# Kernel tuning notes

Hardware: AMD Instinct MI355X
Metric: run time of the kernel (lower is better)

Reference implementation:

```python
import jax, jax.numpy as jnp
import numpy as np

N_QUBITS = 8
N_LAYERS = 4
BATCH = 4096


def _ry(theta):
    # RY(theta) = [[cos(t/2), -sin(t/2)], [sin(t/2), cos(t/2)]]
    c = jnp.cos(theta / 2).astype(jnp.complex64)
    s = jnp.sin(theta / 2).astype(jnp.complex64)
    return jnp.stack([jnp.stack([c, -s], axis=-1),
                      jnp.stack([s, c], axis=-1)], axis=-2)  # (..., 2, 2)


def _rz(theta):
    # RZ(theta) = diag(exp(-i t/2), exp(+i t/2))
    p = jnp.exp(-0.5j * theta.astype(jnp.complex64))
    z = jnp.zeros_like(p)
    return jnp.stack([jnp.stack([p, z], axis=-1),
                      jnp.stack([z, jnp.conj(p)], axis=-1)], axis=-2)


def _apply_1q(state, U, w):
    # state: (B, 2, 2, ..., 2); apply 2x2 unitary U on wire w (axis 1+w).
    st = jnp.moveaxis(state, 1 + w, -1)
    if U.ndim == 3:  # per-sample (batched) gate, U: (B, 2, 2)
        st = jnp.einsum('bij,b...j->b...i', U, st)
    else:            # shared gate, U: (2, 2)
        st = jnp.einsum('ij,b...j->b...i', U, st)
    return jnp.moveaxis(st, -1, 1 + w)


def _apply_cnot(state, c, t):
    # flip target wire t where control wire c is |1>
    st = jnp.moveaxis(state, (1 + c, 1 + t), (-2, -1))
    st = jnp.concatenate([st[..., 0:1, :], st[..., 1:2, ::-1]], axis=-2)
    return jnp.moveaxis(st, (-2, -1), (1 + c, 1 + t))


def _circuit(x, weights):
    B = x.shape[0]
    state = jnp.zeros((B,) + (2,) * N_QUBITS, jnp.complex64)
    state = state.at[(slice(None),) + (0,) * N_QUBITS].set(1.0)  # |0...0>
    # Angle encoding: RY(x_i) on each wire, batched over samples
    for i in range(N_QUBITS):
        state = _apply_1q(state, _ry(x[:, i]), i)
    # Variational layers: CNOT ring then RY/RZ rotations
    for l in range(N_LAYERS):
        for i in range(N_QUBITS):
            state = _apply_cnot(state, i, (i + 1) % N_QUBITS)
        for i in range(N_QUBITS):
            state = _apply_1q(state, _ry(weights[l, i, 0]), i)
            state = _apply_1q(state, _rz(weights[l, i, 1]), i)
    # <Z_0> = P(q0=0) - P(q0=1)
    probs = jnp.sum(jnp.abs(state.reshape(B, 2, -1)) ** 2, axis=-1)
    return (probs[:, 0] - probs[:, 1]).astype(jnp.float32)


def setup_inputs() -> dict:
    key = jax.random.key(0)
    k1, k2 = jax.random.split(key)
    x = jax.random.uniform(k1, (BATCH, N_QUBITS), dtype=jnp.float32) * jnp.pi
    weights = jax.random.normal(k2, (N_LAYERS, N_QUBITS, 2), dtype=jnp.float32) * 0.1
    return {"x": x, "weights": weights}


def reference(x, weights):
    return _circuit(x, weights)
```

## Files before the change

### kernel.cpp

```cpp
#include <hip/hip_runtime.h>

#define NQ 8
#define NL 4
#define BATCH 4096


template <int CTRL>
__device__ __forceinline__ float dppx(float v) {
  return __int_as_float(
      __builtin_amdgcn_update_dpp(0, __float_as_int(v), CTRL, 0xF, 0xF, true));
}

template <int MASK>
__device__ __forceinline__ float swzx(float v) {
  return __int_as_float(
      __builtin_amdgcn_ds_swizzle(__float_as_int(v), (MASK << 10) | 0x1F));
}

__device__ __forceinline__ float xor32(float v) { return __shfl_xor(v, 32, 64); }

template <int W>
__device__ __forceinline__ float xl(float v) {
  if constexpr (W == 0) return xor32(v);
  else if constexpr (W == 1) return swzx<16>(v);
  else if constexpr (W == 2) return dppx<0x128>(v);
  else if constexpr (W == 3) return swzx<4>(v);
  else if constexpr (W == 4) return dppx<0x4E>(v);
  else return dppx<0xB1>(v);
}

template <int W>
__device__ __forceinline__ void ry_gate(float re[4], float im[4],
                                        float c, float s, int lane) {
  if constexpr (W <= 5) {
    const float ss = ((lane >> (5 - W)) & 1) ? s : -s;
    float pr[4], pi[4];
#pragma unroll
    for (int r = 0; r < 4; ++r) { pr[r] = xl<W>(re[r]); pi[r] = xl<W>(im[r]); }
#pragma unroll
    for (int r = 0; r < 4; ++r) {
      re[r] = c * re[r] + ss * pr[r];
      im[r] = c * im[r] + ss * pi[r];
    }
  } else {
    constexpr int m = (W == 6) ? 2 : 1;
#pragma unroll
    for (int r = 0; r < 4; ++r) {
      if ((r & m) == 0) {
        const int r1 = r | m;
        float a0r = re[r], a1r = re[r1], a0i = im[r], a1i = im[r1];
        re[r]  = c * a0r - s * a1r;  re[r1] = s * a0r + c * a1r;
        im[r]  = c * a0i - s * a1i;  im[r1] = s * a0i + c * a1i;
      }
    }
  }
}

template <int W>
__device__ __forceinline__ void rz_gate(float re[4], float im[4],
                                        float c, float s, int lane) {
  if constexpr (W <= 5) {
    const float ss = ((lane >> (5 - W)) & 1) ? s : -s;
#pragma unroll
    for (int r = 0; r < 4; ++r) {
      float nr = re[r] * c - im[r] * ss;
      float ni = im[r] * c + re[r] * ss;
      re[r] = nr; im[r] = ni;
    }
  } else {
    constexpr int m = (W == 6) ? 2 : 1;
#pragma unroll
    for (int r = 0; r < 4; ++r) {
      const float ss = (r & m) ? s : -s;
      float nr = re[r] * c - im[r] * ss;
      float ni = im[r] * c + re[r] * ss;
      re[r] = nr; im[r] = ni;
    }
  }
}

template <int W>
__device__ __forceinline__ void cnot_lane(float re[4], float im[4], bool p) {
  float pr[4], pi[4];
#pragma unroll
  for (int r = 0; r < 4; ++r) { pr[r] = xl<W>(re[r]); pi[r] = xl<W>(im[r]); }
#pragma unroll
  for (int r = 0; r < 4; ++r) {
    re[r] = p ? pr[r] : re[r];
    im[r] = p ? pi[r] : im[r];
  }
}

__device__ __forceinline__ void cnot_ring(float re[4], float im[4], int lane) {
  cnot_lane<1>(re, im, (lane & 32) != 0);
  cnot_lane<2>(re, im, (lane & 16) != 0);
  cnot_lane<3>(re, im, (lane & 8) != 0);
  cnot_lane<4>(re, im, (lane & 4) != 0);
  cnot_lane<5>(re, im, (lane & 2) != 0);
  {
    const bool p = (lane & 1) != 0;
#pragma unroll
    for (int r = 0; r < 2; ++r) {
      float t0 = re[r], t1 = re[r + 2];
      re[r] = p ? t1 : t0; re[r + 2] = p ? t0 : t1;
      t0 = im[r]; t1 = im[r + 2];
      im[r] = p ? t1 : t0; im[r + 2] = p ? t0 : t1;
    }
  }
  { float t = re[2]; re[2] = re[3]; re[3] = t;
    t = im[2]; im[2] = im[3]; im[3] = t; }
  re[1] = xor32(re[1]); im[1] = xor32(im[1]);
  re[3] = xor32(re[3]); im[3] = xor32(im[3]);
}

__global__ __launch_bounds__(256) void vqc_kernel(const float* __restrict__ x,
                                                  const float* __restrict__ w,
                                                  float* __restrict__ out) {
  const int lane = (int)(threadIdx.x & 63);
  const int s = (int)((blockIdx.x * blockDim.x + threadIdx.x) >> 6);

  float re[4], im[4];
#pragma unroll
  for (int r = 0; r < 4; ++r) { re[r] = 0.f; im[r] = 0.f; }
  if (lane == 0) re[0] = 1.f;

  {
    const float4 x0 = *(const float4*)&x[s * 8];
    const float4 x1 = *(const float4*)&x[s * 8 + 4];
    float c, sn;
    __sincosf(x0.x * 0.5f, &sn, &c); ry_gate<0>(re, im, c, sn, lane);
    __sincosf(x0.y * 0.5f, &sn, &c); ry_gate<1>(re, im, c, sn, lane);
    __sincosf(x0.z * 0.5f, &sn, &c); ry_gate<2>(re, im, c, sn, lane);
    __sincosf(x0.w * 0.5f, &sn, &c); ry_gate<3>(re, im, c, sn, lane);
    __sincosf(x1.x * 0.5f, &sn, &c); ry_gate<4>(re, im, c, sn, lane);
    __sincosf(x1.y * 0.5f, &sn, &c); ry_gate<5>(re, im, c, sn, lane);
    __sincosf(x1.z * 0.5f, &sn, &c); ry_gate<6>(re, im, c, sn, lane);
    __sincosf(x1.w * 0.5f, &sn, &c); ry_gate<7>(re, im, c, sn, lane);
  }

#pragma unroll
  for (int l = 0; l < NL; ++l) {
    cnot_ring(re, im, lane);
    const float* wl = &w[l * NQ * 2];
#define APPLY_ROT(W) { float cy, sy, cz, sz;            \
    __sincosf(wl[(W) * 2 + 0] * 0.5f, &sy, &cy);        \
    __sincosf(wl[(W) * 2 + 1] * 0.5f, &sz, &cz);        \
    ry_gate<W>(re, im, cy, sy, lane);                   \
    rz_gate<W>(re, im, cz, sz, lane); }
    APPLY_ROT(0) APPLY_ROT(1) APPLY_ROT(2) APPLY_ROT(3)
    APPLY_ROT(4) APPLY_ROT(5) APPLY_ROT(6) APPLY_ROT(7)
#undef APPLY_ROT
  }

  float acc = 0.f;
#pragma unroll
  for (int r = 0; r < 4; ++r) acc += re[r] * re[r] + im[r] * im[r];
  acc = (lane & 32) ? -acc : acc;
  acc += dppx<0xB1>(acc);
  acc += dppx<0x4E>(acc);
  acc += swzx<4>(acc);
  acc += dppx<0x128>(acc);
  acc += swzx<16>(acc);
  acc += xor32(acc);
  if (lane == 0) out[s] = acc;
}

extern "C" void kernel_launch(void* const* d_in, const int* in_sizes, int n_in,
                              void* d_out, int out_size, void* d_ws, size_t ws_size,
                              hipStream_t stream) {
  const float* x = (const float*)d_in[0];
  const float* w = (const float*)d_in[1];
  float* out = (float*)d_out;
  (void)in_sizes; (void)n_in; (void)out_size; (void)d_ws; (void)ws_size;

  dim3 grid(BATCH / 4), block(256);
  hipLaunchKernelGGL(vqc_kernel, grid, block, 0, stream, x, w, out);
}
```

Before: 67.22 us.

## Pack two samples per wavefront with 8 amplitudes per lane

New measurement: 66.55 us. No clear change (-1.0%).

```diff
diff --git a/kernel.cpp b/kernel.cpp
--- a/kernel.cpp
+++ b/kernel.cpp
@@ -4,6 +4,15 @@
 #define NL 4
 #define BATCH 4096
 
+
+#define INV_4PI 0.07957747154594767f
+
+__device__ __forceinline__ float half_sin(float t) {
+  return __builtin_amdgcn_sinf(t * INV_4PI);
+}
+__device__ __forceinline__ float half_cos(float t) {
+  return __builtin_amdgcn_cosf(t * INV_4PI);
+}
 
 template <int CTRL>
 __device__ __forceinline__ float dppx(float v) {
@@ -17,152 +26,173 @@
       __builtin_amdgcn_ds_swizzle(__float_as_int(v), (MASK << 10) | 0x1F));
 }
 
-__device__ __forceinline__ float xor32(float v) { return __shfl_xor(v, 32, 64); }
-
-template <int W>
-__device__ __forceinline__ float xl(float v) {
-  if constexpr (W == 0) return xor32(v);
-  else if constexpr (W == 1) return swzx<16>(v);
-  else if constexpr (W == 2) return dppx<0x128>(v);
-  else if constexpr (W == 3) return swzx<4>(v);
-  else if constexpr (W == 4) return dppx<0x4E>(v);
+template <int W>
+__device__ __forceinline__ float xl(float v, int lane) {
+  if constexpr (W == 3) return swzx<16>(v);
+  else if constexpr (W == 4) return dppx<0x128>(v);
+  else if constexpr (W == 5) {
+    float lo = dppx<0x104>(v);
+    float hi = dppx<0x114>(v);
+    return (lane & 4) ? hi : lo;
+  }
+  else if constexpr (W == 6) return dppx<0x4E>(v);
   else return dppx<0xB1>(v);
 }
 
 template <int W>
-__device__ __forceinline__ void ry_gate(float re[4], float im[4],
+__device__ __forceinline__ void ry_reg(float re[8], float im[8], float c, float s) {
+  constexpr int m = 4 >> W;
+#pragma unroll
+  for (int r = 0; r < 8; ++r) {
+    if ((r & m) == 0) {
+      const int r1 = r | m;
+      float a0r = re[r], a1r = re[r1], a0i = im[r], a1i = im[r1];
+      re[r]  = c * a0r - s * a1r;  re[r1] = s * a0r + c * a1r;
+      im[r]  = c * a0i - s * a1i;  im[r1] = s * a0i + c * a1i;
+    }
+  }
+}
+
+template <int W>
+__device__ __forceinline__ void ry_lane(float re[8], float im[8],
                                         float c, float s, int lane) {
-  if constexpr (W <= 5) {
-    const float ss = ((lane >> (5 - W)) & 1) ? s : -s;
-    float pr[4], pi[4];
-#pragma unroll
-    for (int r = 0; r < 4; ++r) { pr[r] = xl<W>(re[r]); pi[r] = xl<W>(im[r]); }
-#pragma unroll
-    for (int r = 0; r < 4; ++r) {
-      re[r] = c * re[r] + ss * pr[r];
-      im[r] = c * im[r] + ss * pi[r];
-    }
-  } else {
-    constexpr int m = (W == 6) ? 2 : 1;
-#pragma unroll
-    for (int r = 0; r < 4; ++r) {
-      if ((r & m) == 0) {
-        const int r1 = r | m;
-        float a0r = re[r], a1r = re[r1], a0i = im[r], a1i = im[r1];
-        re[r]  = c * a0r - s * a1r;  re[r1] = s * a0r + c * a1r;
-        im[r]  = c * a0i - s * a1i;  im[r1] = s * a0i + c * a1i;
-      }
-    }
-  }
-}
-
-template <int W>
-__device__ __forceinline__ void rz_gate(float re[4], float im[4],
+  const float ss = ((lane >> (7 - W)) & 1) ? s : -s;
+#pragma unroll
+  for (int r = 0; r < 8; ++r) {
+    float pr = xl<W>(re[r], lane);
+    float pi = xl<W>(im[r], lane);
+    re[r] = c * re[r] + ss * pr;
+    im[r] = c * im[r] + ss * pi;
+  }
+}
+
+template <int W>
+__device__ __forceinline__ void rz_reg(float re[8], float im[8], float c, float s) {
+  constexpr int m = 4 >> W;
+#pragma unroll
+  for (int r = 0; r < 8; ++r) {
+    const float ss = (r & m) ? s : -s;
+    float nr = c * re[r] - ss * im[r];
+    float ni = c * im[r] + ss * re[r];
+    re[r] = nr; im[r] = ni;
+  }
+}
+
+template <int W>
+__device__ __forceinline__ void rz_lane(float re[8], float im[8],
                                         float c, float s, int lane) {
-  if constexpr (W <= 5) {
-    const float ss = ((lane >> (5 - W)) & 1) ? s : -s;
-#pragma unroll
-    for (int r = 0; r < 4; ++r) {
-      float nr = re[r] * c - im[r] * ss;
-      float ni = im[r] * c + re[r] * ss;
-      re[r] = nr; im[r] = ni;
-    }
-  } else {
-    constexpr int m = (W == 6) ? 2 : 1;
-#pragma unroll
-    for (int r = 0; r < 4; ++r) {
-      const float ss = (r & m) ? s : -s;
-      float nr = re[r] * c - im[r] * ss;
-      float ni = im[r] * c + re[r] * ss;
-      re[r] = nr; im[r] = ni;
-    }
-  }
-}
-
-template <int W>
-__device__ __forceinline__ void cnot_lane(float re[4], float im[4], bool p) {
-  float pr[4], pi[4];
-#pragma unroll
-  for (int r = 0; r < 4; ++r) { pr[r] = xl<W>(re[r]); pi[r] = xl<W>(im[r]); }
-#pragma unroll
-  for (int r = 0; r < 4; ++r) {
-    re[r] = p ? pr[r] : re[r];
-    im[r] = p ? pi[r] : im[r];
-  }
-}
-
-__device__ __forceinline__ void cnot_ring(float re[4], float im[4], int lane) {
-  cnot_lane<1>(re, im, (lane & 32) != 0);
-  cnot_lane<2>(re, im, (lane & 16) != 0);
-  cnot_lane<3>(re, im, (lane & 8) != 0);
-  cnot_lane<4>(re, im, (lane & 4) != 0);
-  cnot_lane<5>(re, im, (lane & 2) != 0);
+  const float ss = ((lane >> (7 - W)) & 1) ? s : -s;
+#pragma unroll
+  for (int r = 0; r < 8; ++r) {
+    float nr = c * re[r] - ss * im[r];
+    float ni = c * im[r] + ss * re[r];
+    re[r] = nr; im[r] = ni;
+  }
+}
+
+template <int W>
+__device__ __forceinline__ void cnot_lane(float re[8], float im[8],
+                                          bool p, int lane) {
+#pragma unroll
+  for (int r = 0; r < 8; ++r) {
+    float pr = xl<W>(re[r], lane);
+    float pi = xl<W>(im[r], lane);
+    re[r] = p ? pr : re[r];
+    im[r] = p ? pi : im[r];
+  }
+}
+
+__device__ __forceinline__ void cnot_ring(float re[8], float im[8], int lane) {
+  { float t;
+    t = re[4]; re[4] = re[6]; re[6] = t;  t = im[4]; im[4] = im[6]; im[6] = t;
+    t = re[5]; re[5] = re[7]; re[7] = t;  t = im[5]; im[5] = im[7]; im[7] = t; }
+  { float t;
+    t = re[2]; re[2] = re[3]; re[3] = t;  t = im[2]; im[2] = im[3]; im[3] = t;
+    t = re[6]; re[6] = re[7]; re[7] = t;  t = im[6]; im[6] = im[7]; im[7] = t; }
+#pragma unroll
+  for (int r = 1; r < 8; r += 2) {
+    re[r] = swzx<16>(re[r]);
+    im[r] = swzx<16>(im[r]);
+  }
+  cnot_lane<4>(re, im, (lane & 16) != 0, lane);
+  cnot_lane<5>(re, im, (lane & 8) != 0, lane);
+  cnot_lane<6>(re, im, (lane & 4) != 0, lane);
+  cnot_lane<7>(re, im, (lane & 2) != 0, lane);
   {
     const bool p = (lane & 1) != 0;
 #pragma unroll
-    for (int r = 0; r < 2; ++r) {
-      float t0 = re[r], t1 = re[r + 2];
-      re[r] = p ? t1 : t0; re[r + 2] = p ? t0 : t1;
-      t0 = im[r]; t1 = im[r + 2];
-      im[r] = p ? t1 : t0; im[r + 2] = p ? t0 : t1;
+    for (int r = 0; r < 4; ++r) {
+      float t0 = re[r], t1 = re[r + 4];
+      re[r] = p ? t1 : t0; re[r + 4] = p ? t0 : t1;
+      t0 = im[r]; t1 = im[r + 4];
+      im[r] = p ? t1 : t0; im[r + 4] = p ? t0 : t1;
     }
   }
-  { float t = re[2]; re[2] = re[3]; re[3] = t;
-    t = im[2]; im[2] = im[3]; im[3] = t; }
-  re[1] = xor32(re[1]); im[1] = xor32(im[1]);
-  re[3] = xor32(re[3]); im[3] = xor32(im[3]);
 }
 
 __global__ __launch_bounds__(256) void vqc_kernel(const float* __restrict__ x,
                                                   const float* __restrict__ w,
                                                   float* __restrict__ out) {
   const int lane = (int)(threadIdx.x & 63);
-  const int s = (int)((blockIdx.x * blockDim.x + threadIdx.x) >> 6);
-
-  float re[4], im[4];
-#pragma unroll
-  for (int r = 0; r < 4; ++r) { re[r] = 0.f; im[r] = 0.f; }
-  if (lane == 0) re[0] = 1.f;
+  const int wv = (int)((blockIdx.x * blockDim.x + threadIdx.x) >> 6);
+  const int s = wv * 2 + (lane >> 5);
+
+  float re[8], im[8];
+#pragma unroll
+  for (int r = 0; r < 8; ++r) { re[r] = 0.f; im[r] = 0.f; }
+  if ((lane & 31) == 0) re[0] = 1.f;
 
   {
     const float4 x0 = *(const float4*)&x[s * 8];
     const float4 x1 = *(const float4*)&x[s * 8 + 4];
-    float c, sn;
-    __sincosf(x0.x * 0.5f, &sn, &c); ry_gate<0>(re, im, c, sn, lane);
-    __sincosf(x0.y * 0.5f, &sn, &c); ry_gate<1>(re, im, c, sn, lane);
-    __sincosf(x0.z * 0.5f, &sn, &c); ry_gate<2>(re, im, c, sn, lane);
-    __sincosf(x0.w * 0.5f, &sn, &c); ry_gate<3>(re, im, c, sn, lane);
-    __sincosf(x1.x * 0.5f, &sn, &c); ry_gate<4>(re, im, c, sn, lane);
-    __sincosf(x1.y * 0.5f, &sn, &c); ry_gate<5>(re, im, c, sn, lane);
-    __sincosf(x1.z * 0.5f, &sn, &c); ry_gate<6>(re, im, c, sn, lane);
-    __sincosf(x1.w * 0.5f, &sn, &c); ry_gate<7>(re, im, c, sn, lane);
-  }
-
-#pragma unroll
+    const float t[8] = {x0.x, x0.y, x0.z, x0.w, x1.x, x1.y, x1.z, x1.w};
+    float cs[8], sn[8];
+#pragma unroll
+    for (int i = 0; i < 8; ++i) { sn[i] = half_sin(t[i]); cs[i] = half_cos(t[i]); }
+    ry_reg<0>(re, im, cs[0], sn[0]);
+    ry_reg<1>(re, im, cs[1], sn[1]);
+    ry_reg<2>(re, im, cs[2], sn[2]);
+    ry_lane<3>(re, im, cs[3], sn[3], lane);
+    ry_lane<4>(re, im, cs[4], sn[4], lane);
+    ry_lane<5>(re, im, cs[5], sn[5], lane);
+    ry_lane<6>(re, im, cs[6], sn[6], lane);
+    ry_lane<7>(re, im, cs[7], sn[7], lane);
+  }
+
+#pragma unroll 1
   for (int l = 0; l < NL; ++l) {
     cnot_ring(re, im, lane);
     const float* wl = &w[l * NQ * 2];
-#define APPLY_ROT(W) { float cy, sy, cz, sz;            \
-    __sincosf(wl[(W) * 2 + 0] * 0.5f, &sy, &cy);        \
-    __sincosf(wl[(W) * 2 + 1] * 0.5f, &sz, &cz);        \
-    ry_gate<W>(re, im, cy, sy, lane);                   \
-    rz_gate<W>(re, im, cz, sz, lane); }
-    APPLY_ROT(0) APPLY_ROT(1) APPLY_ROT(2) APPLY_ROT(3)
-    APPLY_ROT(4) APPLY_ROT(5) APPLY_ROT(6) APPLY_ROT(7)
-#undef APPLY_ROT
+    float cy[8], sy[8], cz[8], sz[8];
+#pragma unroll
+    for (int i = 0; i < 8; ++i) {
+      float ty = wl[i * 2 + 0];
+      float tz = wl[i * 2 + 1];
+      sy[i] = half_sin(ty); cy[i] = half_cos(ty);
+      sz[i] = half_sin(tz); cz[i] = half_cos(tz);
+    }
+    ry_reg<0>(re, im, cy[0], sy[0]);        rz_reg<0>(re, im, cz[0], sz[0]);
+    ry_reg<1>(re, im, cy[1], sy[1]);        rz_reg<1>(re, im, cz[1], sz[1]);
+    ry_reg<2>(re, im, cy[2], sy[2]);        rz_reg<2>(re, im, cz[2], sz[2]);
+    ry_lane<3>(re, im, cy[3], sy[3], lane); rz_lane<3>(re, im, cz[3], sz[3], lane);
+    ry_lane<4>(re, im, cy[4], sy[4], lane); rz_lane<4>(re, im, cz[4], sz[4], lane);
+    ry_lane<5>(re, im, cy[5], sy[5], lane); rz_lane<5>(re, im, cz[5], sz[5], lane);
+    ry_lane<6>(re, im, cy[6], sy[6], lane); rz_lane<6>(re, im, cz[6], sz[6], lane);
+    ry_lane<7>(re, im, cy[7], sy[7], lane); rz_lane<7>(re, im, cz[7], sz[7], lane);
   }
 
   float acc = 0.f;
 #pragma unroll
-  for (int r = 0; r < 4; ++r) acc += re[r] * re[r] + im[r] * im[r];
-  acc = (lane & 32) ? -acc : acc;
+  for (int r = 0; r < 8; ++r) {
+    float m2 = re[r] * re[r] + im[r] * im[r];
+    acc += (r & 4) ? -m2 : m2;
+  }
   acc += dppx<0xB1>(acc);
   acc += dppx<0x4E>(acc);
   acc += swzx<4>(acc);
   acc += dppx<0x128>(acc);
   acc += swzx<16>(acc);
-  acc += xor32(acc);
-  if (lane == 0) out[s] = acc;
+  if ((lane & 31) == 0) out[s] = acc;
 }
 
 extern "C" void kernel_launch(void* const* d_in, const int* in_sizes, int n_in,
@@ -173,6 +203,6 @@
   float* out = (float*)d_out;
   (void)in_sizes; (void)n_in; (void)out_size; (void)d_ws; (void)ws_size;
 
-  dim3 grid(BATCH / 4), block(256);
+  dim3 grid(BATCH / 8), block(256);
   hipLaunchKernelGGL(vqc_kernel, grid, block, 0, stream, x, w, out);
 }
```
